# Optimization experiments

Measured on AMD Instinct MI355X. Metric: run time of the kernel, lower is better.

## Reference

```python
import jax, jax.numpy as jnp
import numpy as np

N_POINTS = 4096
N_PROJS = 2000


def setup_inputs() -> dict:
    key = jax.random.key(0)
    k1, k2, k3 = jax.random.split(key, 3)
    Xs = jax.random.normal(k1, (N_POINTS, 3), dtype=jnp.float32)
    Xt = jax.random.normal(k2, (N_POINTS, 3), dtype=jnp.float32)
    Us = jax.random.normal(k3, (N_PROJS, 3, 2), dtype=jnp.float32)
    return {"Xs": Xs, "Xt": Xt, "Us": Us}


def _project_to_circle(X, Us):
    # X: [n, d], Us: [P, d, 2] -> angles in [0, 1): [P, n]
    Xp = jnp.einsum('pdk,nd->pnk', Us, X)  # [P, n, 2]
    nrm = jnp.sqrt(jnp.sum(Xp * Xp, axis=-1, keepdims=True))
    Xp = Xp / jnp.maximum(nrm, 1e-12)  # F.normalize
    return (jnp.arctan2(-Xp[..., 1], -Xp[..., 0]) + np.pi) / (2 * np.pi)


def _emd1d_circle_p1(u_values, v_values):
    # Circular W1 via level-median (Delon et al.). u,v: [P, n], [P, m]
    P, n = u_values.shape
    m = v_values.shape[-1]
    dt = u_values.dtype
    u_w = jnp.full((P, n), 1.0 / n, dtype=dt)
    v_w = jnp.full((P, m), 1.0 / m, dtype=dt)
    us = jnp.sort(u_values, axis=-1)
    vs = jnp.sort(v_values, axis=-1)
    vals = jnp.concatenate([us, vs], axis=-1)            # [P, n+m]
    sorter = jnp.argsort(vals, axis=-1)
    vals_sorted = jnp.take_along_axis(vals, sorter, axis=-1)
    w_cat = jnp.concatenate([u_w, -v_w], axis=-1)
    cdf_diff = jnp.cumsum(jnp.take_along_axis(w_cat, sorter, axis=-1), axis=-1)
    cdf_sorter = jnp.argsort(cdf_diff, axis=-1)
    cdf_diff_sorted = jnp.take_along_axis(cdf_diff, cdf_sorter, axis=-1)
    vals_pad = jnp.concatenate([vals_sorted, jnp.ones((P, 1), dtype=dt)], axis=-1)
    delta = vals_pad[..., 1:] - vals_pad[..., :-1]
    weight_sorted = jnp.take_along_axis(delta, cdf_sorter, axis=-1)
    sum_weights = jnp.cumsum(weight_sorted, axis=-1) - 0.5
    sum_weights = jnp.where(sum_weights < 0, jnp.inf, sum_weights)
    inds = jnp.argmin(sum_weights, axis=-1)
    levMed = jnp.take_along_axis(cdf_diff_sorted, inds[:, None], axis=-1)  # [P, 1]
    return jnp.sum(delta * jnp.abs(cdf_diff - levMed), axis=-1)  # [P]


def reference(Xs, Xt, Us):
    Xps = _project_to_circle(Xs, Us)  # [P, n]
    Xpt = _project_to_circle(Xt, Us)  # [P, m]
    w1 = _emd1d_circle_p1(Xps, Xpt)
    return jnp.mean(w1)
```

## Files before the change

### kernel.cpp

```cpp
#include <hip/hip_runtime.h>
#include <math.h>

#define NPTS   4096
#define NPROJ  2000
#define NB     256
#define NMERGE 8192
#define VPT    32

__device__ __forceinline__ int sw(int i) {
    return (i & ~31) | ((i + (i >> 5)) & 31);
}

__device__ __forceinline__ void local_merge(float v[VPT], bool asc) {
    #pragma unroll
    for (int j = VPT / 2; j >= 1; j >>= 1) {
        #pragma unroll
        for (int e = 0; e < VPT; ++e) {
            if ((e & j) == 0) {
                float a = v[e], b = v[e | j];
                float mn = fminf(a, b), mx = fmaxf(a, b);
                v[e]     = asc ? mn : mx;
                v[e | j] = asc ? mx : mn;
            }
        }
    }
}

__global__ __launch_bounds__(NB) void swd_kernel(
    const float* __restrict__ Xs, const float* __restrict__ Xt,
    const float* __restrict__ Us, float* __restrict__ out)
{
    __shared__ float keys[NMERGE];
    __shared__ float red[15 * 4];

    const int tid  = threadIdx.x;
    const int arr  = tid >> 7;
    const int c    = tid & 127;
    const int lane = tid & 63;
    const int wid  = tid >> 6;
    const int p    = blockIdx.x;

    const float u00 = Us[p*6+0], u01 = Us[p*6+1];
    const float u10 = Us[p*6+2], u11 = Us[p*6+3];
    const float u20 = Us[p*6+4], u21 = Us[p*6+5];

    const float pi_f   = 3.14159265358979323846f;
    const float inv2pi = 0.15915494309189535f;

    const float* __restrict__ X = arr ? Xt : Xs;

    float v[VPT];
    {
        const float4* X4 = (const float4*)(X + c * (VPT * 3));
        #pragma unroll
        for (int t = 0; t < 8; ++t) {
            float4 q0 = X4[t*3+0], q1 = X4[t*3+1], q2 = X4[t*3+2];
            #define ANG(x,y,z) ((atan2f(-((x)*u01+(y)*u11+(z)*u21), \
                                        -((x)*u00+(y)*u10+(z)*u20)) + pi_f) * inv2pi)
            v[t*4+0] = ANG(q0.x, q0.y, q0.z);
            v[t*4+1] = ANG(q0.w, q1.x, q1.y);
            v[t*4+2] = ANG(q1.z, q1.w, q2.x);
            v[t*4+3] = ANG(q2.y, q2.z, q2.w);
            #undef ANG
            __builtin_amdgcn_sched_barrier(0);
        }
    }

    #pragma unroll
    for (int k = 2; k <= 16; k <<= 1) {
        #pragma unroll
        for (int j = k >> 1; j >= 1; j >>= 1) {
            #pragma unroll
            for (int e = 0; e < VPT; ++e) {
                if ((e & j) == 0) {
                    bool asc = ((e & k) == 0);
                    float a = v[e], b = v[e | j];
                    float mn = fminf(a, b), mx = fmaxf(a, b);
                    v[e]     = asc ? mn : mx;
                    v[e | j] = asc ? mx : mn;
                }
            }
        }
    }

    local_merge(v, (c & 1) == 0);

    #pragma unroll
    for (int k = 64; k <= 2048; k <<= 1) {
        bool asc = ((c & (k >> 5)) == 0);
        #pragma unroll
        for (int d = k >> 6; d >= 1; d >>= 1) {
            bool keepmin = (((c & d) == 0) == asc);
            #pragma unroll
            for (int e = 0; e < VPT; ++e) {
                float o = __shfl_xor(v[e], d, 64);
                v[e] = keepmin ? fminf(v[e], o) : fmaxf(v[e], o);
            }
        }
        local_merge(v, asc);
    }

    #pragma unroll
    for (int e = 0; e < VPT; ++e) keys[sw(tid * VPT + e)] = v[e];
    __syncthreads();
    {
        const int pb = (tid ^ 64) * VPT;
        const bool keepmin = (c & 64) == 0;
        #pragma unroll
        for (int e = 0; e < VPT; ++e) {
            float o = keys[sw(pb + e)];
            v[e] = keepmin ? fminf(v[e], o) : fmaxf(v[e], o);
        }
    }
    __syncthreads();
    #pragma unroll
    for (int d = 32; d >= 1; d >>= 1) {
        bool keepmin = ((c & d) == 0);
        #pragma unroll
        for (int e = 0; e < VPT; ++e) {
            float o = __shfl_xor(v[e], d, 64);
            v[e] = keepmin ? fminf(v[e], o) : fmaxf(v[e], o);
        }
    }
    local_merge(v, true);

    #pragma unroll
    for (int e = 0; e < VPT; ++e) keys[sw(tid * VPT + e)] = v[e];
    __syncthreads();

    int c_init;
    unsigned int c8[8] = {0,0,0,0,0,0,0,0};
    {
        const int d0 = tid * VPT;
        int lo = d0 > NPTS ? d0 - NPTS : 0;
        int hi = d0 < NPTS ? d0 : NPTS;
        while (lo < hi) {
            int mid = (lo + hi) >> 1;
            if (keys[sw(mid)] <= keys[sw(NPTS + (d0 - 1 - mid))]) lo = mid + 1; else hi = mid;
        }
        int i = lo, j = d0 - lo;
        c_init = i - j;
        const float FMAXV = 3.402823466e+38f;
        float cu = (i < NPTS) ? keys[sw(i)] : FMAXV;
        float cv = (j < NPTS) ? keys[sw(NPTS + j)] : FMAXV;
        #pragma unroll
        for (int s = 0; s < VPT; ++s) {
            float cur;
            if (cu <= cv) { cur = cu; ++i; cu = (i < NPTS) ? keys[sw(i)] : FMAXV; }
            else          { cur = cv; ++j; cv = (j < NPTS) ? keys[sw(NPTS + j)] : FMAXV; }
            float nxt = fminf(cu, cv);
            if (nxt == FMAXV) nxt = 1.0f;
            v[s] = nxt - cur;
            int off = (i - j) - c_init;
            c8[s >> 2] |= ((unsigned int)(off & 0xff)) << ((s & 3) * 8);
        }
    }

    int lo_c = -4097, hi_c = 4096;
    #pragma unroll 1
    for (int it = 0; it < 14; ++it) {
        const int mid = (lo_c + hi_c) >> 1;
        const int thr = mid - c_init;
        float s_loc = 0.0f;
        #pragma unroll
        for (int s = 0; s < VPT; ++s) {
            int off = (int)(c8[s >> 2] << ((3 - (s & 3)) * 8)) >> 24;
            s_loc += (off <= thr) ? v[s] : 0.0f;
        }
        #pragma unroll
        for (int o = 32; o >= 1; o >>= 1) s_loc += __shfl_down(s_loc, o, 64);
        if (lane == 0) red[it * 4 + wid] = s_loc;
        __syncthreads();
        float S = red[it*4+0] + red[it*4+1] + red[it*4+2] + red[it*4+3];
        if (S >= 0.5f) hi_c = mid; else lo_c = mid;
    }
    const int cstar = hi_c;

    float part = 0.0f;
    {
        const int thr = cstar - c_init;
        #pragma unroll
        for (int s = 0; s < VPT; ++s) {
            int off = (int)(c8[s >> 2] << ((3 - (s & 3)) * 8)) >> 24;
            part += v[s] * fabsf((float)(off - thr));
        }
    }
    #pragma unroll
    for (int o = 32; o >= 1; o >>= 1) part += __shfl_down(part, o, 64);
    if (lane == 0) red[56 + wid] = part;
    __syncthreads();
    if (tid == 0) {
        float w1 = (red[56] + red[57] + red[58] + red[59]) * (1.0f / 4096.0f);
        atomicAdd(out, w1 * (1.0f / (float)NPROJ));
    }
}

extern "C" void kernel_launch(void* const* d_in, const int* in_sizes, int n_in,
                              void* d_out, int out_size, void* d_ws, size_t ws_size,
                              hipStream_t stream) {
    const float* Xs = (const float*)d_in[0];
    const float* Xt = (const float*)d_in[1];
    const float* Us = (const float*)d_in[2];
    float* out = (float*)d_out;

    hipMemsetAsync(out, 0, sizeof(float), stream);
    swd_kernel<<<NPROJ, NB, 0, stream>>>(Xs, Xt, Us, out);
}
```

Before: 258.0 us.

## Replace level-median binary search with shared-memory histogram over CDF levels

Instead of 14 iterations of block-wide reductions with barriers to find the weighted median CDF level, each merged gap is atomically added into a 2048-bin shared histogram keyed by CDF offset. A single prefix scan then finds the median bin, and the final cost is computed from the histogram. If any offset falls outside the bin range, the kernel falls back to a recomputing binary search. It also adds a launch_bounds occupancy hint, and it trades the per-iteration barriers for shared-memory float atomics, which may contend and change summation order.

```diff
diff --git a/kernel.cpp b/kernel.cpp
--- a/kernel.cpp
+++ b/kernel.cpp
@@ -6,6 +6,8 @@
 #define NB     256
 #define NMERGE 8192
 #define VPT    32
+#define HBINS  2048
+#define HOFF   1024
 
 __device__ __forceinline__ int sw(int i) {
     return (i & ~31) | ((i + (i >> 5)) & 31);
@@ -26,12 +28,15 @@
     }
 }
 
-__global__ __launch_bounds__(NB) void swd_kernel(
+__global__ __launch_bounds__(NB, 4) void swd_kernel(
     const float* __restrict__ Xs, const float* __restrict__ Xt,
     const float* __restrict__ Us, float* __restrict__ out)
 {
     __shared__ float keys[NMERGE];
-    __shared__ float red[15 * 4];
+    __shared__ float hist[HBINS];
+    __shared__ float wsum[4];
+    __shared__ int   s_cstar;
+    __shared__ int   s_oor;
 
     const int tid  = threadIdx.x;
     const int arr  = tid >> 7;
@@ -66,6 +71,9 @@
         }
     }
 
+    for (int i = tid; i < HBINS; i += NB) hist[i] = 0.0f;
+    if (tid == 0) { s_cstar = HBINS - 1; s_oor = 0; }
+
     #pragma unroll
     for (int k = 2; k <= 16; k <<= 1) {
         #pragma unroll
@@ -128,8 +136,7 @@
     for (int e = 0; e < VPT; ++e) keys[sw(tid * VPT + e)] = v[e];
     __syncthreads();
 
-    int c_init;
-    unsigned int c8[8] = {0,0,0,0,0,0,0,0};
+    int lo0;
     {
         const int d0 = tid * VPT;
         int lo = d0 > NPTS ? d0 - NPTS : 0;
@@ -138,11 +145,12 @@
             int mid = (lo + hi) >> 1;
             if (keys[sw(mid)] <= keys[sw(NPTS + (d0 - 1 - mid))]) lo = mid + 1; else hi = mid;
         }
+        lo0 = lo;
         int i = lo, j = d0 - lo;
-        c_init = i - j;
         const float FMAXV = 3.402823466e+38f;
         float cu = (i < NPTS) ? keys[sw(i)] : FMAXV;
         float cv = (j < NPTS) ? keys[sw(NPTS + j)] : FMAXV;
+        bool oor = false;
         #pragma unroll
         for (int s = 0; s < VPT; ++s) {
             float cur;
@@ -150,48 +158,112 @@
             else          { cur = cv; ++j; cv = (j < NPTS) ? keys[sw(NPTS + j)] : FMAXV; }
             float nxt = fminf(cu, cv);
             if (nxt == FMAXV) nxt = 1.0f;
-            v[s] = nxt - cur;
-            int off = (i - j) - c_init;
-            c8[s >> 2] |= ((unsigned int)(off & 0xff)) << ((s & 3) * 8);
-        }
-    }
-
-    int lo_c = -4097, hi_c = 4096;
-    #pragma unroll 1
-    for (int it = 0; it < 14; ++it) {
-        const int mid = (lo_c + hi_c) >> 1;
-        const int thr = mid - c_init;
-        float s_loc = 0.0f;
-        #pragma unroll
+            int b  = (i - j) + HOFF;
+            int bc = b < 0 ? 0 : (b > HBINS - 1 ? HBINS - 1 : b);
+            oor |= (b != bc);
+            atomicAdd(&hist[bc], nxt - cur);
+        }
+        if (oor) s_oor = 1;
+    }
+    __syncthreads();
+
+    if (s_oor == 0) {
+        const int base = tid * (HBINS / NB);
+        float colsum = 0.0f;
+        #pragma unroll
+        for (int k = 0; k < HBINS / NB; ++k) colsum += hist[base + k];
+
+        float ps = colsum;
+        #pragma unroll
+        for (int o = 1; o < 64; o <<= 1) {
+            float t2 = __shfl_up(ps, o, 64);
+            if (lane >= o) ps += t2;
+        }
+        if (lane == 63) wsum[wid] = ps;
+        __syncthreads();
+        float wbase = 0.0f;
+        #pragma unroll
+        for (int w = 0; w < 4; ++w) wbase += (w < wid) ? wsum[w] : 0.0f;
+        float incl = wbase + ps;
+        float excl = incl - colsum;
+        if (incl >= 0.5f && excl < 0.5f + 1e-6f) {
+            float run = excl;
+            int found = base + (HBINS / NB) - 1;
+            #pragma unroll
+            for (int k = 0; k < HBINS / NB; ++k) {
+                run += hist[base + k];
+                if (run >= 0.5f) { found = base + k; break; }
+            }
+            atomicMin(&s_cstar, found);
+        }
+        __syncthreads();
+        const int cb = s_cstar;
+
+        float part = 0.0f;
+        #pragma unroll
+        for (int k = 0; k < HBINS / NB; ++k) {
+            int b = base + k;
+            part += hist[b] * fabsf((float)(b - cb));
+        }
+        #pragma unroll
+        for (int o = 32; o >= 1; o >>= 1) part += __shfl_down(part, o, 64);
+        if (lane == 0) wsum[wid] = part;
+        __syncthreads();
+        if (tid == 0) {
+            float w1 = (wsum[0] + wsum[1] + wsum[2] + wsum[3]) * (1.0f / 4096.0f);
+            atomicAdd(out, w1 * (1.0f / (float)NPROJ));
+        }
+    } else {
+        const int d0 = tid * VPT;
+        const float FMAXV = 3.402823466e+38f;
+        int lo_c = -4097, hi_c = 4096;
+        #pragma unroll 1
+        for (int it = 0; it < 14; ++it) {
+            const int mid = (lo_c + hi_c) >> 1;
+            int i = lo0, j = d0 - lo0;
+            float cu = (i < NPTS) ? keys[sw(i)] : FMAXV;
+            float cv = (j < NPTS) ? keys[sw(NPTS + j)] : FMAXV;
+            float s_loc = 0.0f;
+            #pragma unroll 1
+            for (int s = 0; s < VPT; ++s) {
+                float cur;
+                if (cu <= cv) { cur = cu; ++i; cu = (i < NPTS) ? keys[sw(i)] : FMAXV; }
+                else          { cur = cv; ++j; cv = (j < NPTS) ? keys[sw(NPTS + j)] : FMAXV; }
+                float nxt = fminf(cu, cv);
+                if (nxt == FMAXV) nxt = 1.0f;
+                if ((i - j) <= mid) s_loc += nxt - cur;
+            }
+            #pragma unroll
+            for (int o = 32; o >= 1; o >>= 1) s_loc += __shfl_down(s_loc, o, 64);
+            __syncthreads();
+            if (lane == 0) wsum[wid] = s_loc;
+            __syncthreads();
+            float S = wsum[0] + wsum[1] + wsum[2] + wsum[3];
+            if (S >= 0.5f) hi_c = mid; else lo_c = mid;
+        }
+        const int cs = hi_c;
+        int i = lo0, j = d0 - lo0;
+        float cu = (i < NPTS) ? keys[sw(i)] : FMAXV;
+        float cv = (j < NPTS) ? keys[sw(NPTS + j)] : FMAXV;
+        float part = 0.0f;
+        #pragma unroll 1
         for (int s = 0; s < VPT; ++s) {
-            int off = (int)(c8[s >> 2] << ((3 - (s & 3)) * 8)) >> 24;
-            s_loc += (off <= thr) ? v[s] : 0.0f;
-        }
-        #pragma unroll
-        for (int o = 32; o >= 1; o >>= 1) s_loc += __shfl_down(s_loc, o, 64);
-        if (lane == 0) red[it * 4 + wid] = s_loc;
-        __syncthreads();
-        float S = red[it*4+0] + red[it*4+1] + red[it*4+2] + red[it*4+3];
-        if (S >= 0.5f) hi_c = mid; else lo_c = mid;
-    }
-    const int cstar = hi_c;
-
-    float part = 0.0f;
-    {
-        const int thr = cstar - c_init;
-        #pragma unroll
-        for (int s = 0; s < VPT; ++s) {
-            int off = (int)(c8[s >> 2] << ((3 - (s & 3)) * 8)) >> 24;
-            part += v[s] * fabsf((float)(off - thr));
-        }
-    }
-    #pragma unroll
-    for (int o = 32; o >= 1; o >>= 1) part += __shfl_down(part, o, 64);
-    if (lane == 0) red[56 + wid] = part;
-    __syncthreads();
-    if (tid == 0) {
-        float w1 = (red[56] + red[57] + red[58] + red[59]) * (1.0f / 4096.0f);
-        atomicAdd(out, w1 * (1.0f / (float)NPROJ));
+            float cur;
+            if (cu <= cv) { cur = cu; ++i; cu = (i < NPTS) ? keys[sw(i)] : FMAXV; }
+            else          { cur = cv; ++j; cv = (j < NPTS) ? keys[sw(NPTS + j)] : FMAXV; }
+            float nxt = fminf(cu, cv);
+            if (nxt == FMAXV) nxt = 1.0f;
+            part += (nxt - cur) * fabsf((float)((i - j) - cs));
+        }
+        #pragma unroll
+        for (int o = 32; o >= 1; o >>= 1) part += __shfl_down(part, o, 64);
+        __syncthreads();
+        if (lane == 0) wsum[wid] = part;
+        __syncthreads();
+        if (tid == 0) {
+            float w1 = (wsum[0] + wsum[1] + wsum[2] + wsum[3]) * (1.0f / 4096.0f);
+            atomicAdd(out, w1 * (1.0f / (float)NPROJ));
+        }
     }
 }
 
```

Result: slower. 271.6 us (+5.3%).
